# Kernel tuning notes

Measured on AMD Instinct MI355X. Metric: run time of the kernel, lower is better.

Reference implementation:

```python
import jax, jax.numpy as jnp
import numpy as np

BN_EPS = 1e-5


def setup_inputs() -> dict:
    key = jax.random.key(0)
    ks = jax.random.split(key, 6)
    B, C, K, N = 4, 64, 16, 16384  # batch, feat channels, neighbors, points
    W_OUT = 16  # weightnet output channels (fixed by Linear(16*mlp[-1], ...))
    xyz = jax.random.normal(ks[0], (B, N, 3), dtype=jnp.float32)
    points = jax.random.normal(ks[1], (B, C, K, N), dtype=jnp.float32)
    coordinate = jax.random.normal(ks[2], (B, 3, K, N), dtype=jnp.float32)
    w1 = jax.random.normal(ks[3], (W_OUT, 3), dtype=jnp.float32) * 0.5
    b1 = jnp.zeros((W_OUT,), dtype=jnp.float32)
    lin_w = jax.random.normal(ks[4], (C, W_OUT * C), dtype=jnp.float32) * (1.0 / np.sqrt(W_OUT * C))
    lin_b = jnp.zeros((C,), dtype=jnp.float32)
    gamma = jnp.ones((C,), dtype=jnp.float32)
    beta = jnp.zeros((C,), dtype=jnp.float32)
    return {"xyz": xyz, "points": points, "coordinate": coordinate,
            "w1": w1, "b1": b1, "lin_w": lin_w, "lin_b": lin_b,
            "gamma": gamma, "beta": beta}


def reference(xyz, points, coordinate, w1, b1, lin_w, lin_b, gamma, beta):
    B, C, K, N = points.shape
    # weightnet: 1x1 conv (3 -> 16) + ReLU over coordinate [B,3,K,N] -> [B,16,K,N]
    weights = jax.nn.relu(jnp.einsum('oc,bckn->bokn', w1, coordinate) + b1[None, :, None, None])
    # per-point aggregation: [B,N,C,K] @ [B,N,K,16] -> [B,N,C,16]
    new_points = jnp.einsum('bckn,bokn->bnco', points, weights)
    new_points = new_points.reshape(B, N, C * 16)  # [B, N, 16*C]
    # linear projection 16*C -> C
    new_points = jnp.einsum('bnk,ok->bno', new_points, lin_w) + lin_b  # [B, N, C]
    # BatchNorm1d over channel dim (training-mode batch stats), layout [B, C, N]
    new_points = new_points.transpose(0, 2, 1)  # [B, C, N]
    mean = jnp.mean(new_points, axis=(0, 2), keepdims=True)
    var = jnp.var(new_points, axis=(0, 2), keepdims=True)
    new_points = (new_points - mean) * jax.lax.rsqrt(var + BN_EPS)
    new_points = new_points * gamma[None, :, None] + beta[None, :, None]
    new_points = jax.nn.relu(new_points)  # [B, C, N]
    return (xyz, new_points)
```

## Files before the change

kernel.cpp:

```cpp
#include <hip/hip_runtime.h>

#define BB 4
#define CC 64
#define KK 16
#define NN 16384
#define NTB 128

typedef __attribute__((ext_vector_type(8))) short short8;
typedef __attribute__((ext_vector_type(4))) float floatx4;
typedef __attribute__((ext_vector_type(2))) _Float16 half2v;

__device__ __forceinline__ unsigned short f2bf_rtne(float x) {
    unsigned u = __builtin_bit_cast(unsigned, x);
    u += 0x7FFFu + ((u >> 16) & 1u);
    return (unsigned short)(u >> 16);
}

__device__ __forceinline__ unsigned pack_bf16x2(float lo, float hi) {
    unsigned a = __builtin_bit_cast(unsigned, lo) + 0x8000u;
    unsigned b = __builtin_bit_cast(unsigned, hi) + 0x8000u;
    return __builtin_amdgcn_perm(b, a, 0x07060302u);
}

__device__ __forceinline__ half2v cvt2h(float a, float b) {
    return __builtin_bit_cast(half2v, __builtin_amdgcn_cvt_pkrtz(a, b));
}

#if __has_builtin(__builtin_amdgcn_fdot2)
#define DOT2(a, b, c) __builtin_amdgcn_fdot2((a), (b), (c), false)
#else
__device__ __forceinline__ float dot2_fb(half2v a, half2v b, float c) {
    return fmaf((float)a[0], (float)b[0], fmaf((float)a[1], (float)b[1], c));
}
#define DOT2(a, b, c) dot2_fb((a), (b), (c))
#endif

__global__ __launch_bounds__(256)
void prep_bfrag(const float* __restrict__ lin_w, unsigned short* __restrict__ bfrag,
                float* __restrict__ part)
{
    const int tid  = blockIdx.x * 256 + threadIdx.x;
    if (tid < 512) part[tid] = 0.0f;

    const int lane = tid & 63;
    const int g    = tid >> 6;
    const int ci   = g >> 4;
    const int kk   = (g >> 2) & 3;
    const int nt   = g & 3;
    const int r    = lane & 15;
    const int sq   = lane >> 4;

    const float* src = lin_w + (size_t)(nt * 16 + r) * 1024 + ci * 128 + kk * 32 + sq * 8;
    unsigned short v[8];
    #pragma unroll
    for (int j = 0; j < 8; ++j) v[j] = f2bf_rtne(src[j]);
    *(uint4*)(bfrag + ((size_t)g * 64 + lane) * 8) = *(const uint4*)v;
}

__global__ __launch_bounds__(256, 2)
void fused_main(const float* __restrict__ points,
                const float* __restrict__ coordinate,
                const float* __restrict__ w1,
                const float* __restrict__ b1,
                const unsigned short* __restrict__ bfrag,
                float* __restrict__ y_out,
                float* __restrict__ part)
{
    __shared__ uint4 s_a[2][2][4 * 257];

    const int t    = threadIdx.x;
    const int lane = t & 63;
    const int wv   = __builtin_amdgcn_readfirstlane(t >> 6);
    const int P    = wv >> 1;
    const int h    = wv & 1;
    const int r    = lane & 15;
    const int sq   = lane >> 4;

    const int bid = blockIdx.x;
    const int b   = bid >> 7;
    const int n0  = (bid & 127) * NTB + P * 64;

    half2v wh[8][8];
    {
        const float* coordB = coordinate + (size_t)b * 3 * KK * NN + n0 + lane;
        float c0[KK], c1[KK], c2[KK];
        #pragma unroll
        for (int k = 0; k < KK; ++k) {
            c0[k] = coordB[(0 * KK + k) * NN];
            c1[k] = coordB[(1 * KK + k) * NN];
            c2[k] = coordB[(2 * KK + k) * NN];
        }
        #pragma unroll
        for (int j = 0; j < 8; ++j) {
            const int o = 8 * h + j;
            const float w1x = w1[o * 3 + 0];
            const float w1y = w1[o * 3 + 1];
            const float w1z = w1[o * 3 + 2];
            const float bo  = b1[o];
            #pragma unroll
            for (int kp = 0; kp < 8; ++kp) {
                float v0 = fmaf(w1x, c0[2 * kp],     fmaf(w1y, c1[2 * kp],     fmaf(w1z, c2[2 * kp],     bo)));
                float v1 = fmaf(w1x, c0[2 * kp + 1], fmaf(w1y, c1[2 * kp + 1], fmaf(w1z, c2[2 * kp + 1], bo)));
                wh[j][kp] = cvt2h(fmaxf(v0, 0.0f), fmaxf(v1, 0.0f));
            }
        }
    }

    floatx4 acc[2][4];
    #pragma unroll
    for (int m = 0; m < 2; ++m)
        #pragma unroll
        for (int nt = 0; nt < 4; ++nt) acc[m][nt] = (floatx4){0.f, 0.f, 0.f, 0.f};

    const float* pB = points + (size_t)b * CC * KK * NN + n0 + lane;

    float pv[4][16];
    #pragma unroll
    for (int d = 0; d < 4; ++d)
        #pragma unroll
        for (int k = 0; k < KK; ++k)
            pv[d][k] = pB[((size_t)d * KK + k) * NN];

    for (int ci = 0; ci < 8; ++ci) {
        const int buf = ci & 1;
        uint4* saW = &s_a[P][buf][0];
        #pragma unroll
        for (int cl = 0; cl < 8; ++cl) {
            const int cc   = ci * 8 + cl;
            const int slot = cc & 3;
            half2v ph[8];
            #pragma unroll
            for (int kp = 0; kp < 8; ++kp)
                ph[kp] = cvt2h(pv[slot][2 * kp], pv[slot][2 * kp + 1]);
            {
                const int cp = (cc + 4 < CC) ? (cc + 4) : (CC - 1);
                #pragma unroll
                for (int k = 0; k < KK; ++k)
                    pv[slot][k] = pB[((size_t)cp * KK + k) * NN];
            }
            float a8[8];
            #pragma unroll
            for (int j = 0; j < 8; ++j) {
                float a = 0.f;
                #pragma unroll
                for (int kp = 0; kp < 8; ++kp) a = DOT2(ph[kp], wh[j][kp], a);
                a8[j] = a;
            }
            uint4 pk;
            pk.x = pack_bf16x2(a8[0], a8[1]);
            pk.y = pack_bf16x2(a8[2], a8[3]);
            pk.z = pack_bf16x2(a8[4], a8[5]);
            pk.w = pack_bf16x2(a8[6], a8[7]);
            saW[(lane >> 4) * 257 + (cl >> 1) * 64 + (lane & 15) * 4 + (cl & 1) * 2 + h] = pk;
        }

        uint4 bf_c[4];
        #pragma unroll
        for (int nt = 0; nt < 4; ++nt)
            bf_c[nt] = *(const uint4*)(bfrag + ((((size_t)ci * 4 + 0) * 4 + nt) * 64 + lane) * 8);

        asm volatile("s_waitcnt lgkmcnt(0)\n\ts_barrier" ::: "memory");

        const uint4* saR = &s_a[P][buf][0];
        #pragma unroll
        for (int kk = 0; kk < 4; ++kk) {
            uint4 bf_n[4];
            if (kk < 3) {
                #pragma unroll
                for (int nt = 0; nt < 4; ++nt)
                    bf_n[nt] = *(const uint4*)(bfrag + ((((size_t)ci * 4 + kk + 1) * 4 + nt) * 64 + lane) * 8);
            }
            short8 af[2];
            #pragma unroll
            for (int m = 0; m < 2; ++m)
                af[m] = __builtin_bit_cast(short8, saR[(2 * h + m) * 257 + kk * 64 + r * 4 + sq]);
            #pragma unroll
            for (int m = 0; m < 2; ++m)
                #pragma unroll
                for (int nt = 0; nt < 4; ++nt)
                    acc[m][nt] = __builtin_amdgcn_mfma_f32_16x16x32_bf16(
                        af[m], __builtin_bit_cast(short8, bf_c[nt]), acc[m][nt], 0, 0, 0);
            #pragma unroll
            for (int nt = 0; nt < 4; ++nt) bf_c[nt] = bf_n[nt];
        }
    }

    float* yB = y_out + (size_t)b * CC * NN + n0;
    float* sb  = (float*)&s_a[0][0][0];
    float* sb2 = sb + 512;
    #pragma unroll
    for (int m = 0; m < 2; ++m)
        #pragma unroll
        for (int nt = 0; nt < 4; ++nt) {
            const int oc = nt * 16 + r;
            const float4 v = make_float4(acc[m][nt][0], acc[m][nt][1],
                                         acc[m][nt][2], acc[m][nt][3]);
            *(float4*)(yB + (size_t)oc * NN + (2 * h + m) * 16 + sq * 4) = v;

            float s  = v.x + v.y + v.z + v.w;
            float ss = v.x * v.x + v.y * v.y + v.z * v.z + v.w * v.w;
            s  += __shfl_xor(s, 16);  s  += __shfl_xor(s, 32);
            ss += __shfl_xor(ss, 16); ss += __shfl_xor(ss, 32);
            if (lane < 16) {
                sb [(wv * 2 + m) * 64 + oc] = s;
                sb2[(wv * 2 + m) * 64 + oc] = ss;
            }
        }
    __syncthreads();
    if (t < 64) {
        float S = 0.f, SS = 0.f;
        #pragma unroll
        for (int q = 0; q < 8; ++q) {
            S  += sb [q * 64 + t];
            SS += sb2[q * 64 + t];
        }
        atomicAdd(&part[b * 64 + t], S);
        atomicAdd(&part[256 + b * 64 + t], SS);
    }
}

__global__ void bn_stats(const float* __restrict__ part,
                         const float* __restrict__ gamma,
                         const float* __restrict__ beta,
                         float* __restrict__ ab)
{
    const int ch = threadIdx.x;
    float S = 0.f, SS = 0.f;
    #pragma unroll
    for (int b = 0; b < BB; ++b) {
        S  += part[b * 64 + ch];
        SS += part[256 + b * 64 + ch];
    }
    const float inv  = 1.0f / (float)(BB * NN);
    const float mean = S * inv;
    const float var  = SS * inv - mean * mean;
    const float a    = gamma[ch] * rsqrtf(var + 1e-5f);
    ab[ch]      = a;
    ab[CC + ch] = beta[ch] - mean * a;
}

__global__ __launch_bounds__(256)
void bn_apply(float* __restrict__ y, const float* __restrict__ ab)
{
    const size_t i = (size_t)blockIdx.x * 256 + threadIdx.x;
    float4* p = (float4*)y;
    float4 v = p[i];
    const int ch = (int)((i * 4) >> 14) & 63;
    const float a = ab[ch], bb = ab[CC + ch];
    v.x = fmaxf(fmaf(a, v.x, bb), 0.0f);
    v.y = fmaxf(fmaf(a, v.y, bb), 0.0f);
    v.z = fmaxf(fmaf(a, v.z, bb), 0.0f);
    v.w = fmaxf(fmaf(a, v.w, bb), 0.0f);
    p[i] = v;
}

extern "C" void kernel_launch(void* const* d_in, const int* in_sizes, int n_in,
                              void* d_out, int out_size, void* d_ws, size_t ws_size,
                              hipStream_t stream)
{
    const float* xyz        = (const float*)d_in[0];
    const float* points     = (const float*)d_in[1];
    const float* coordinate = (const float*)d_in[2];
    const float* w1         = (const float*)d_in[3];
    const float* b1         = (const float*)d_in[4];
    const float* lin_w      = (const float*)d_in[5];
    const float* gamma      = (const float*)d_in[7];
    const float* beta       = (const float*)d_in[8];

    float* out = (float*)d_out;

    unsigned short* bfrag = (unsigned short*)d_ws;
    float* part = (float*)d_ws + 32768;
    float* ab   = part + 512;

    const size_t xyz_elems = (size_t)BB * NN * 3;
    (void)hipMemcpyAsync(out, xyz, xyz_elems * sizeof(float),
                         hipMemcpyDeviceToDevice, stream);

    float* y_out = out + xyz_elems;

    prep_bfrag<<<32, 256, 0, stream>>>(lin_w, bfrag, part);
    fused_main<<<BB * (NN / NTB), 256, 0, stream>>>(
        points, coordinate, w1, b1, bfrag, y_out, part);
    bn_stats<<<1, 64, 0, stream>>>(part, gamma, beta, ab);
    bn_apply<<<(BB * CC * NN) / 4 / 256, 256, 0, stream>>>(y_out, ab);
}
```

Before: 400.5 us.

## Process two points per lane with float2 loads and swizzled LDS layout

Each lane now handles two adjacent points and loads points and coordinates as float2, so every wave covers all 128 points of the block. In exchange each wave computes only 4 of the 16 weightnet channels, and the per-lane weight registers shrink. The points prefetch depth drops from 4 channels to 2 to hold register pressure steady. Shared memory A-tiles move to a single XOR-swizzled layout with 8-byte stores, replacing the padded layout, and the aim is wider global transactions and fewer LDS bank conflicts. The risk is that the shallower prefetch exposes more memory latency.

After: 432.3 us. 1.08x slower.

```diff
diff --git a/kernel.cpp b/kernel.cpp
--- a/kernel.cpp
+++ b/kernel.cpp
@@ -25,6 +25,8 @@
 __device__ __forceinline__ half2v cvt2h(float a, float b) {
     return __builtin_bit_cast(half2v, __builtin_amdgcn_cvt_pkrtz(a, b));
 }
+
+__device__ __forceinline__ float selp(float2 v, int p) { return p ? v.y : v.x; }
 
 #if __has_builtin(__builtin_amdgcn_fdot2)
 #define DOT2(a, b, c) __builtin_amdgcn_fdot2((a), (b), (c), false)
@@ -66,43 +68,45 @@
                 float* __restrict__ y_out,
                 float* __restrict__ part)
 {
-    __shared__ uint4 s_a[2][2][4 * 257];
+    __shared__ uint4 s_a[2][2048];
 
     const int t    = threadIdx.x;
     const int lane = t & 63;
-    const int wv   = __builtin_amdgcn_readfirstlane(t >> 6);
-    const int P    = wv >> 1;
-    const int h    = wv & 1;
+    const int w    = __builtin_amdgcn_readfirstlane(t >> 6);
     const int r    = lane & 15;
     const int sq   = lane >> 4;
 
     const int bid = blockIdx.x;
     const int b   = bid >> 7;
-    const int n0  = (bid & 127) * NTB + P * 64;
-
-    half2v wh[8][8];
+    const int n0  = (bid & 127) * NTB;
+
+    half2v wh[2][4][8];
     {
-        const float* coordB = coordinate + (size_t)b * 3 * KK * NN + n0 + lane;
-        float c0[KK], c1[KK], c2[KK];
-        #pragma unroll
-        for (int k = 0; k < KK; ++k) {
-            c0[k] = coordB[(0 * KK + k) * NN];
-            c1[k] = coordB[(1 * KK + k) * NN];
-            c2[k] = coordB[(2 * KK + k) * NN];
-        }
-        #pragma unroll
-        for (int j = 0; j < 8; ++j) {
-            const int o = 8 * h + j;
+        const float* coordB = coordinate + (size_t)b * 3 * KK * NN + n0 + 2 * lane;
+        float2 c2[3][KK];
+        #pragma unroll
+        for (int dim = 0; dim < 3; ++dim)
+            #pragma unroll
+            for (int k = 0; k < KK; ++k)
+                c2[dim][k] = *(const float2*)(coordB + ((size_t)dim * KK + k) * NN);
+        #pragma unroll
+        for (int j = 0; j < 4; ++j) {
+            const int o = 4 * w + j;
             const float w1x = w1[o * 3 + 0];
             const float w1y = w1[o * 3 + 1];
             const float w1z = w1[o * 3 + 2];
             const float bo  = b1[o];
             #pragma unroll
-            for (int kp = 0; kp < 8; ++kp) {
-                float v0 = fmaf(w1x, c0[2 * kp],     fmaf(w1y, c1[2 * kp],     fmaf(w1z, c2[2 * kp],     bo)));
-                float v1 = fmaf(w1x, c0[2 * kp + 1], fmaf(w1y, c1[2 * kp + 1], fmaf(w1z, c2[2 * kp + 1], bo)));
-                wh[j][kp] = cvt2h(fmaxf(v0, 0.0f), fmaxf(v1, 0.0f));
-            }
+            for (int p = 0; p < 2; ++p)
+                #pragma unroll
+                for (int kp = 0; kp < 8; ++kp) {
+                    const float x0 = selp(c2[0][2 * kp], p), x1 = selp(c2[0][2 * kp + 1], p);
+                    const float y0 = selp(c2[1][2 * kp], p), y1 = selp(c2[1][2 * kp + 1], p);
+                    const float z0 = selp(c2[2][2 * kp], p), z1 = selp(c2[2][2 * kp + 1], p);
+                    float v0 = fmaf(w1x, x0, fmaf(w1y, y0, fmaf(w1z, z0, bo)));
+                    float v1 = fmaf(w1x, x1, fmaf(w1y, y1, fmaf(w1z, z1, bo)));
+                    wh[p][j][kp] = cvt2h(fmaxf(v0, 0.0f), fmaxf(v1, 0.0f));
+                }
         }
     }
 
@@ -112,46 +116,54 @@
         #pragma unroll
         for (int nt = 0; nt < 4; ++nt) acc[m][nt] = (floatx4){0.f, 0.f, 0.f, 0.f};
 
-    const float* pB = points + (size_t)b * CC * KK * NN + n0 + lane;
-
-    float pv[4][16];
-    #pragma unroll
-    for (int d = 0; d < 4; ++d)
+    const float* pB = points + (size_t)b * CC * KK * NN + n0 + 2 * lane;
+
+    float2 pv[2][KK];
+    #pragma unroll
+    for (int d = 0; d < 2; ++d)
         #pragma unroll
         for (int k = 0; k < KK; ++k)
-            pv[d][k] = pB[((size_t)d * KK + k) * NN];
+            pv[d][k] = *(const float2*)(pB + ((size_t)d * KK + k) * NN);
 
     for (int ci = 0; ci < 8; ++ci) {
         const int buf = ci & 1;
-        uint4* saW = &s_a[P][buf][0];
+        uint4* saW = &s_a[buf][0];
         #pragma unroll
         for (int cl = 0; cl < 8; ++cl) {
             const int cc   = ci * 8 + cl;
-            const int slot = cc & 3;
-            half2v ph[8];
-            #pragma unroll
-            for (int kp = 0; kp < 8; ++kp)
-                ph[kp] = cvt2h(pv[slot][2 * kp], pv[slot][2 * kp + 1]);
+            const int slot = cl & 1;
+            half2v ph[2][8];
+            #pragma unroll
+            for (int p = 0; p < 2; ++p)
+                #pragma unroll
+                for (int kp = 0; kp < 8; ++kp)
+                    ph[p][kp] = cvt2h(selp(pv[slot][2 * kp], p), selp(pv[slot][2 * kp + 1], p));
             {
-                const int cp = (cc + 4 < CC) ? (cc + 4) : (CC - 1);
+                const int cp = (cc + 2 < CC) ? (cc + 2) : (CC - 1);
                 #pragma unroll
                 for (int k = 0; k < KK; ++k)
-                    pv[slot][k] = pB[((size_t)cp * KK + k) * NN];
+                    pv[slot][k] = *(const float2*)(pB + ((size_t)cp * KK + k) * NN);
             }
-            float a8[8];
-            #pragma unroll
-            for (int j = 0; j < 8; ++j) {
-                float a = 0.f;
-                #pragma unroll
-                for (int kp = 0; kp < 8; ++kp) a = DOT2(ph[kp], wh[j][kp], a);
-                a8[j] = a;
+            float a4[2][4];
+            #pragma unroll
+            for (int p = 0; p < 2; ++p)
+                #pragma unroll
+                for (int j = 0; j < 4; ++j) {
+                    float a = 0.f;
+                    #pragma unroll
+                    for (int kp = 0; kp < 8; ++kp) a = DOT2(ph[p][kp], wh[p][j][kp], a);
+                    a4[p][j] = a;
+                }
+            #pragma unroll
+            for (int p = 0; p < 2; ++p) {
+                uint2 pk;
+                pk.x = pack_bf16x2(a4[p][0], a4[p][1]);
+                pk.y = pack_bf16x2(a4[p][2], a4[p][3]);
+                const int rw  = 2 * (lane & 7) + p;
+                const int idx = (lane >> 3) * 256 + (cl >> 1) * 64 + rw * 4
+                              + (((cl & 1) * 2 + (w >> 1)) ^ (lane & 3));
+                *(uint2*)((unsigned*)&saW[idx] + 2 * (w & 1)) = pk;
             }
-            uint4 pk;
-            pk.x = pack_bf16x2(a8[0], a8[1]);
-            pk.y = pack_bf16x2(a8[2], a8[3]);
-            pk.z = pack_bf16x2(a8[4], a8[5]);
-            pk.w = pack_bf16x2(a8[6], a8[7]);
-            saW[(lane >> 4) * 257 + (cl >> 1) * 64 + (lane & 15) * 4 + (cl & 1) * 2 + h] = pk;
         }
 
         uint4 bf_c[4];
@@ -161,7 +173,7 @@
 
         asm volatile("s_waitcnt lgkmcnt(0)\n\ts_barrier" ::: "memory");
 
-        const uint4* saR = &s_a[P][buf][0];
+        const uint4* saR = &s_a[buf][0];
         #pragma unroll
         for (int kk = 0; kk < 4; ++kk) {
             uint4 bf_n[4];
@@ -173,7 +185,8 @@
             short8 af[2];
             #pragma unroll
             for (int m = 0; m < 2; ++m)
-                af[m] = __builtin_bit_cast(short8, saR[(2 * h + m) * 257 + kk * 64 + r * 4 + sq]);
+                af[m] = __builtin_bit_cast(short8,
+                    saR[(2 * w + m) * 256 + kk * 64 + r * 4 + (sq ^ ((r >> 1) & 3))]);
             #pragma unroll
             for (int m = 0; m < 2; ++m)
                 #pragma unroll
@@ -186,7 +199,7 @@
     }
 
     float* yB = y_out + (size_t)b * CC * NN + n0;
-    float* sb  = (float*)&s_a[0][0][0];
+    float* sb  = (float*)&s_a[0][0];
     float* sb2 = sb + 512;
     #pragma unroll
     for (int m = 0; m < 2; ++m)
@@ -195,15 +208,15 @@
             const int oc = nt * 16 + r;
             const float4 v = make_float4(acc[m][nt][0], acc[m][nt][1],
                                          acc[m][nt][2], acc[m][nt][3]);
-            *(float4*)(yB + (size_t)oc * NN + (2 * h + m) * 16 + sq * 4) = v;
+            *(float4*)(yB + (size_t)oc * NN + (2 * w + m) * 16 + sq * 4) = v;
 
             float s  = v.x + v.y + v.z + v.w;
             float ss = v.x * v.x + v.y * v.y + v.z * v.z + v.w * v.w;
             s  += __shfl_xor(s, 16);  s  += __shfl_xor(s, 32);
             ss += __shfl_xor(ss, 16); ss += __shfl_xor(ss, 32);
             if (lane < 16) {
-                sb [(wv * 2 + m) * 64 + oc] = s;
-                sb2[(wv * 2 + m) * 64 + oc] = ss;
+                sb [(2 * w + m) * 64 + oc] = s;
+                sb2[(2 * w + m) * 64 + oc] = ss;
             }
         }
     __syncthreads();
```

## Stage points through shared memory with cooperative float4 loads and larger blocks

Applied to the files above, without the earlier changes.

Doubles the point tile per block to 256 with 512 threads. Instead of each lane issuing 16 strided scalar loads per channel into registers, waves cooperatively load float4 rows of points, convert them to fp16 pairs and stage them in a double-buffered LDS array. Each wave then reads its k-pairs from LDS. The goal is wider, coalesced global loads and lower register pressure from the pv prefetch array, at the cost of extra LDS traffic and a block barrier every channel pair.

New measurement: 395.7 us, median of 2. About the same (-1.2%).

```diff
diff --git a/kernel.cpp b/kernel.cpp
--- a/kernel.cpp
+++ b/kernel.cpp
@@ -4,7 +4,7 @@
 #define CC 64
 #define KK 16
 #define NN 16384
-#define NTB 128
+#define NTB 256
 
 typedef __attribute__((ext_vector_type(8))) short short8;
 typedef __attribute__((ext_vector_type(4))) float floatx4;
@@ -24,6 +24,9 @@
 
 __device__ __forceinline__ half2v cvt2h(float a, float b) {
     return __builtin_bit_cast(half2v, __builtin_amdgcn_cvt_pkrtz(a, b));
+}
+__device__ __forceinline__ unsigned pk2u(float a, float b) {
+    return __builtin_bit_cast(unsigned, __builtin_amdgcn_cvt_pkrtz(a, b));
 }
 
 #if __has_builtin(__builtin_amdgcn_fdot2)
@@ -57,7 +60,7 @@
     *(uint4*)(bfrag + ((size_t)g * 64 + lane) * 8) = *(const uint4*)v;
 }
 
-__global__ __launch_bounds__(256, 2)
+__global__ __launch_bounds__(512, 2)
 void fused_main(const float* __restrict__ points,
                 const float* __restrict__ coordinate,
                 const float* __restrict__ w1,
@@ -66,7 +69,8 @@
                 float* __restrict__ y_out,
                 float* __restrict__ part)
 {
-    __shared__ uint4 s_a[2][2][4 * 257];
+    __shared__ unsigned int s_p[2][2][8][256];
+    __shared__ uint4 s_a[4][2][1024];
 
     const int t    = threadIdx.x;
     const int lane = t & 63;
@@ -77,12 +81,13 @@
     const int sq   = lane >> 4;
 
     const int bid = blockIdx.x;
-    const int b   = bid >> 7;
-    const int n0  = (bid & 127) * NTB + P * 64;
+    const int b   = bid >> 6;
+    const int n0b = (bid & 63) * NTB;
+    const int n0p = n0b + P * 64;
 
     half2v wh[8][8];
     {
-        const float* coordB = coordinate + (size_t)b * 3 * KK * NN + n0 + lane;
+        const float* coordB = coordinate + (size_t)b * 3 * KK * NN + n0p + lane;
         float c0[KK], c1[KK], c2[KK];
         #pragma unroll
         for (int k = 0; k < KK; ++k) {
@@ -112,93 +117,120 @@
         #pragma unroll
         for (int nt = 0; nt < 4; ++nt) acc[m][nt] = (floatx4){0.f, 0.f, 0.f, 0.f};
 
-    const float* pB = points + (size_t)b * CC * KK * NN + n0 + lane;
-
-    float pv[4][16];
-    #pragma unroll
-    for (int d = 0; d < 4; ++d)
-        #pragma unroll
-        for (int k = 0; k < KK; ++k)
-            pv[d][k] = pB[((size_t)d * KK + k) * NN];
+    const float* pS = points + (size_t)b * CC * KK * NN + n0b + 4 * lane;
+
+    float4 stF[2][2][2];
+
+#define ISSUE(SLOT, G) {                                                        \
+        const int cA = 2 * (G);                                                 \
+        stF[SLOT][0][0] = *(const float4*)(pS + (size_t)(cA * 16 + 2 * wv) * NN);       \
+        stF[SLOT][0][1] = *(const float4*)(pS + (size_t)(cA * 16 + 2 * wv + 1) * NN);   \
+        stF[SLOT][1][0] = *(const float4*)(pS + (size_t)((cA + 1) * 16 + 2 * wv) * NN); \
+        stF[SLOT][1][1] = *(const float4*)(pS + (size_t)((cA + 1) * 16 + 2 * wv + 1) * NN); }
+
+#define WRITE(SLOT, BUF) {                                                      \
+        _Pragma("unroll")                                                       \
+        for (int ch = 0; ch < 2; ++ch) {                                        \
+            const float4 A = stF[SLOT][ch][0], Bv = stF[SLOT][ch][1];           \
+            uint4 W;                                                            \
+            W.x = pk2u(A.x, Bv.x);  W.y = pk2u(A.y, Bv.y);                      \
+            W.z = pk2u(A.z, Bv.z);  W.w = pk2u(A.w, Bv.w);                      \
+            *(uint4*)&s_p[BUF][ch][wv][4 * lane] = W;                           \
+        } }
+
+#define CONSUME(GEXPR, BUF, GG) {                                               \
+        const int g_ = (GEXPR);                                                 \
+        _Pragma("unroll")                                                       \
+        for (int chh = 0; chh < 2; ++chh) {                                     \
+            const int cl = (2 * (GG) + chh) & 7;    \
+            half2v ph[8];                                                       \
+            _Pragma("unroll")                                                   \
+            for (int kp = 0; kp < 8; ++kp)                                      \
+                ph[kp] = __builtin_bit_cast(half2v, s_p[BUF][chh][kp][P * 64 + lane]); \
+            float a8[8];                                                        \
+            _Pragma("unroll")                                                   \
+            for (int j = 0; j < 8; ++j) {                                       \
+                float a = 0.f;                                                  \
+                _Pragma("unroll")                                               \
+                for (int kp = 0; kp < 8; ++kp) a = DOT2(ph[kp], wh[j][kp], a);  \
+                a8[j] = a;                                                      \
+            }                                                                   \
+            uint4 pk;                                                           \
+            pk.x = pack_bf16x2(a8[0], a8[1]);                                   \
+            pk.y = pack_bf16x2(a8[2], a8[3]);                                   \
+            pk.z = pack_bf16x2(a8[4], a8[5]);                                   \
+            pk.w = pack_bf16x2(a8[6], a8[7]);                                   \
+            s_a[P][((2 * g_ + chh) >> 3) & 1]                                   \
+               [(lane >> 4) * 256 + (cl >> 1) * 64 + (lane & 15) * 4            \
+                + (cl & 1) * 2 + h] = pk;                                       \
+        } }
+
+    ISSUE(0, 0)
+    ISSUE(1, 1)
+    WRITE(0, 0)
+    asm volatile("s_waitcnt lgkmcnt(0)\n\ts_barrier" ::: "memory");
 
     for (int ci = 0; ci < 8; ++ci) {
-        const int buf = ci & 1;
-        uint4* saW = &s_a[P][buf][0];
-        #pragma unroll
-        for (int cl = 0; cl < 8; ++cl) {
-            const int cc   = ci * 8 + cl;
-            const int slot = cc & 3;
-            half2v ph[8];
-            #pragma unroll
-            for (int kp = 0; kp < 8; ++kp)
-                ph[kp] = cvt2h(pv[slot][2 * kp], pv[slot][2 * kp + 1]);
-            {
-                const int cp = (cc + 4 < CC) ? (cc + 4) : (CC - 1);
-                #pragma unroll
-                for (int k = 0; k < KK; ++k)
-                    pv[slot][k] = pB[((size_t)cp * KK + k) * NN];
-            }
-            float a8[8];
-            #pragma unroll
-            for (int j = 0; j < 8; ++j) {
-                float a = 0.f;
-                #pragma unroll
-                for (int kp = 0; kp < 8; ++kp) a = DOT2(ph[kp], wh[j][kp], a);
-                a8[j] = a;
-            }
-            uint4 pk;
-            pk.x = pack_bf16x2(a8[0], a8[1]);
-            pk.y = pack_bf16x2(a8[2], a8[3]);
-            pk.z = pack_bf16x2(a8[4], a8[5]);
-            pk.w = pack_bf16x2(a8[6], a8[7]);
-            saW[(lane >> 4) * 257 + (cl >> 1) * 64 + (lane & 15) * 4 + (cl & 1) * 2 + h] = pk;
-        }
-
-        uint4 bf_c[4];
-        #pragma unroll
-        for (int nt = 0; nt < 4; ++nt)
-            bf_c[nt] = *(const uint4*)(bfrag + ((((size_t)ci * 4 + 0) * 4 + nt) * 64 + lane) * 8);
-
-        asm volatile("s_waitcnt lgkmcnt(0)\n\ts_barrier" ::: "memory");
-
-        const uint4* saR = &s_a[P][buf][0];
-        #pragma unroll
-        for (int kk = 0; kk < 4; ++kk) {
-            uint4 bf_n[4];
-            if (kk < 3) {
+        #pragma unroll
+        for (int gg = 0; gg < 4; ++gg) {
+            const int g = ci * 4 + gg;
+            if (g + 2 < 32) ISSUE(gg & 1, g + 2)
+            CONSUME(g, gg & 1, gg)
+            if (g + 1 < 32) WRITE((gg + 1) & 1, (gg + 1) & 1)
+
+            if (gg == 3) {
+                uint4 bf_c[4];
                 #pragma unroll
                 for (int nt = 0; nt < 4; ++nt)
-                    bf_n[nt] = *(const uint4*)(bfrag + ((((size_t)ci * 4 + kk + 1) * 4 + nt) * 64 + lane) * 8);
+                    bf_c[nt] = *(const uint4*)(bfrag + ((((size_t)ci * 4 + 0) * 4 + nt) * 64 + lane) * 8);
+
+                asm volatile("s_waitcnt lgkmcnt(0)\n\ts_barrier" ::: "memory");
+
+                const uint4* saR = &s_a[P][ci & 1][0];
+                #pragma unroll
+                for (int kk = 0; kk < 4; ++kk) {
+                    uint4 bf_n[4];
+                    if (kk < 3) {
+                        #pragma unroll
+                        for (int nt = 0; nt < 4; ++nt)
+                            bf_n[nt] = *(const uint4*)(bfrag + ((((size_t)ci * 4 + kk + 1) * 4 + nt) * 64 + lane) * 8);
+                    }
+                    short8 af[2];
+                    #pragma unroll
+                    for (int m = 0; m < 2; ++m)
+                        af[m] = __builtin_bit_cast(short8, saR[(2 * h + m) * 256 + kk * 64 + r * 4 + sq]);
+                    #pragma unroll
+                    for (int m = 0; m < 2; ++m)
+                        #pragma unroll
+                        for (int nt = 0; nt < 4; ++nt)
+                            acc[m][nt] = __builtin_amdgcn_mfma_f32_16x16x32_bf16(
+                                af[m], __builtin_bit_cast(short8, bf_c[nt]), acc[m][nt], 0, 0, 0);
+                    #pragma unroll
+                    for (int nt = 0; nt < 4; ++nt) bf_c[nt] = bf_n[nt];
+                }
+            } else {
+                asm volatile("s_waitcnt lgkmcnt(0)\n\ts_barrier" ::: "memory");
             }
-            short8 af[2];
-            #pragma unroll
-            for (int m = 0; m < 2; ++m)
-                af[m] = __builtin_bit_cast(short8, saR[(2 * h + m) * 257 + kk * 64 + r * 4 + sq]);
-            #pragma unroll
-            for (int m = 0; m < 2; ++m)
-                #pragma unroll
-                for (int nt = 0; nt < 4; ++nt)
-                    acc[m][nt] = __builtin_amdgcn_mfma_f32_16x16x32_bf16(
-                        af[m], __builtin_bit_cast(short8, bf_c[nt]), acc[m][nt], 0, 0, 0);
-            #pragma unroll
-            for (int nt = 0; nt < 4; ++nt) bf_c[nt] = bf_n[nt];
         }
     }
-
-    float* yB = y_out + (size_t)b * CC * NN + n0;
-    float* sb  = (float*)&s_a[0][0][0];
-    float* sb2 = sb + 512;
+#undef ISSUE
+#undef WRITE
+#undef CONSUME
+
+    float* yB  = y_out + (size_t)b * CC * NN + n0p;
+    float* sb  = (float*)&s_p[0][0][0][0];
+    float* sb2 = sb + 1024;
     #pragma unroll
     for (int m = 0; m < 2; ++m)
         #pragma unroll
         for (int nt = 0; nt < 4; ++nt) {
             const int oc = nt * 16 + r;
-            const float4 v = make_float4(acc[m][nt][0], acc[m][nt][1],
-                                         acc[m][nt][2], acc[m][nt][3]);
-            *(float4*)(yB + (size_t)oc * NN + (2 * h + m) * 16 + sq * 4) = v;
-
-            float s  = v.x + v.y + v.z + v.w;
-            float ss = v.x * v.x + v.y * v.y + v.z * v.z + v.w * v.w;
+            const floatx4 v = acc[m][nt];
+            *(float4*)(yB + (size_t)oc * NN + (2 * h + m) * 16 + sq * 4) =
+                make_float4(v[0], v[1], v[2], v[3]);
+
+            float s  = v[0] + v[1] + v[2] + v[3];
+            float ss = v[0] * v[0] + v[1] * v[1] + v[2] * v[2] + v[3] * v[3];
             s  += __shfl_xor(s, 16);  s  += __shfl_xor(s, 32);
             ss += __shfl_xor(ss, 16); ss += __shfl_xor(ss, 32);
             if (lane < 16) {
@@ -210,7 +242,7 @@
     if (t < 64) {
         float S = 0.f, SS = 0.f;
         #pragma unroll
-        for (int q = 0; q < 8; ++q) {
+        for (int q = 0; q < 16; ++q) {
             S  += sb [q * 64 + t];
             SS += sb2[q * 64 + t];
         }
@@ -280,7 +312,7 @@
     float* y_out = out + xyz_elems;
 
     prep_bfrag<<<32, 256, 0, stream>>>(lin_w, bfrag, part);
-    fused_main<<<BB * (NN / NTB), 256, 0, stream>>>(
+    fused_main<<<BB * (NN / NTB), 512, 0, stream>>>(
         points, coordinate, w1, b1, bfrag, y_out, part);
     bn_stats<<<1, 64, 0, stream>>>(part, gamma, beta, ab);
     bn_apply<<<(BB * CC * NN) / 4 / 256, 256, 0, stream>>>(y_out, ab);
```
